# Performance work log

Measured on AMD Instinct MI355X. Metric: run time of the kernel, lower is better.

Reference implementation:

```python
import jax, jax.numpy as jnp
import numpy as np

H = 1024
NH = 16
HD = H // NH
EPS = 1e-5

def setup_inputs() -> dict:
    key = jax.random.key(0)
    ks = jax.random.split(key, 5)
    B, S = 2, 2048
    scale = 1.0 / np.sqrt(H)
    return {
        "x": jax.random.normal(ks[0], (B, S, H), dtype=jnp.float32),
        "Wq": jax.random.normal(ks[1], (H, H), dtype=jnp.float32) * scale,
        "Wk": jax.random.normal(ks[2], (H, H), dtype=jnp.float32) * scale,
        "Wv": jax.random.normal(ks[3], (H, H), dtype=jnp.float32) * scale,
        "Wo": jax.random.normal(ks[4], (H, H), dtype=jnp.float32) * scale,
        "bo": jnp.zeros((H,), dtype=jnp.float32),
        "gamma": jnp.ones((H,), dtype=jnp.float32),
        "beta": jnp.zeros((H,), dtype=jnp.float32),
    }

def reference(x, Wq, Wk, Wv, Wo, bo, gamma, beta):
    B, S, _ = x.shape
    residual = x
    # pre-LayerNorm
    mu = jnp.mean(x, axis=-1, keepdims=True)
    var = jnp.mean(jnp.square(x - mu), axis=-1, keepdims=True)
    xn = (x - mu) * jax.lax.rsqrt(var + EPS) * gamma + beta
    # QKV projections (torch Linear: y = x @ W.T), split heads -> [B, NH, S, HD]
    q = (xn @ Wq.T).reshape(B, S, NH, HD).transpose(0, 2, 1, 3)
    k = (xn @ Wk.T).reshape(B, S, NH, HD).transpose(0, 2, 1, 3)
    v = (xn @ Wv.T).reshape(B, S, NH, HD).transpose(0, 2, 1, 3)
    # naive attention: explicit [B, NH, S, S] scores
    scale = 1.0 / np.sqrt(HD)
    scores = jnp.einsum('bhqd,bhkd->bhqk', q, k) * scale
    attn = jax.nn.softmax(scores.astype(jnp.float32), axis=-1).astype(q.dtype)
    out = jnp.einsum('bhqk,bhkd->bhqd', attn, v)
    out = out.transpose(0, 2, 1, 3).reshape(B, S, H)
    out = out @ Wo.T + bo
    return out + residual
```

## Files before the change

### kernel.cpp

```cpp
#include <hip/hip_runtime.h>
#include <hip/hip_bf16.h>

#define H 1024
#define NHEAD 16
#define HDIM 64
#define SEQ 2048
#define BATCH 2
#define M_TOT (BATCH * SEQ)
#define NQKV 3072

typedef __attribute__((ext_vector_type(8))) short bf16x8;
typedef __attribute__((ext_vector_type(4))) float f32x4;

#define C2_SCALE 0.18033688f

__device__ __forceinline__ unsigned short f2bf(float f) {
  union { float f; unsigned int u; } a;
  a.f = f;
  unsigned int u = a.u;
  return (unsigned short)((u + 0x7fffu + ((u >> 16) & 1u)) >> 16);
}

__device__ __forceinline__ unsigned int pkbf(float a, float b) {
  union { __hip_bfloat162 h; unsigned int u; } cv;
  cv.h = __float22bfloat162_rn(float2{a, b});
  return cv.u;
}

__device__ __forceinline__ float fast_exp2(float x) {
#if defined(__has_builtin) && __has_builtin(__builtin_amdgcn_exp2f)
  return __builtin_amdgcn_exp2f(x);
#else
  return exp2f(x);
#endif
}

typedef const __attribute__((address_space(1))) void* gas1_t;
typedef __attribute__((address_space(3))) void* las3_t;
__device__ __forceinline__ void gload16(const void* g, void* l) {
  __builtin_amdgcn_global_load_lds((gas1_t)(unsigned long long)g,
                                   (las3_t)(unsigned int)(unsigned long long)l,
                                   16, 0, 0);
}

__global__ __launch_bounds__(256) void ln_cast_kernel(const float* __restrict__ x,
                                                      const float* __restrict__ gamma,
                                                      const float* __restrict__ beta,
                                                      unsigned short* __restrict__ xn,
                                                      const float* __restrict__ w0,
                                                      const float* __restrict__ w1,
                                                      const float* __restrict__ w2,
                                                      const float* __restrict__ w3,
                                                      unsigned short* __restrict__ wdst) {
  const int t = threadIdx.x;
  if (blockIdx.x >= M_TOT) {
    const int cb = blockIdx.x - M_TOT;
    const int y = cb >> 10;
    const float* s = (y == 0) ? w0 : (y == 1) ? w1 : (y == 2) ? w2 : w3;
    const int i = (cb & 1023) * 256 + t;
    const float4 v = ((const float4*)s)[i];
    ushort4 o;
    o.x = f2bf(v.x);
    o.y = f2bf(v.y);
    o.z = f2bf(v.z);
    o.w = f2bf(v.w);
    ((ushort4*)(wdst + (size_t)y * H * H))[i] = o;
    return;
  }
  const int row = blockIdx.x;
  const float* xr = x + (size_t)row * H;
  float4 v = ((const float4*)xr)[t];
  float s = v.x + v.y + v.z + v.w;
  float s2 = v.x * v.x + v.y * v.y + v.z * v.z + v.w * v.w;
#pragma unroll
  for (int o = 32; o; o >>= 1) {
    s += __shfl_xor(s, o, 64);
    s2 += __shfl_xor(s2, o, 64);
  }
  __shared__ float red[8];
  const int wave = t >> 6;
  if ((t & 63) == 0) {
    red[wave] = s;
    red[wave + 4] = s2;
  }
  __syncthreads();
  const float ts = red[0] + red[1] + red[2] + red[3];
  const float ts2 = red[4] + red[5] + red[6] + red[7];
  const float mu = ts * (1.0f / (float)H);
  const float var = ts2 * (1.0f / (float)H) - mu * mu;
  const float rstd = rsqrtf(var + 1e-5f);
  const float4 g = ((const float4*)gamma)[t];
  const float4 b = ((const float4*)beta)[t];
  ushort4 o;
  o.x = f2bf((v.x - mu) * rstd * g.x + b.x);
  o.y = f2bf((v.y - mu) * rstd * g.y + b.y);
  o.z = f2bf((v.z - mu) * rstd * g.z + b.z);
  o.w = f2bf((v.w - mu) * rstd * g.w + b.w);
  ((ushort4*)(xn + (size_t)row * H))[t] = o;
}

template <int EPI>
__global__ __launch_bounds__(256, 4) void gemm128(const unsigned short* __restrict__ A,
                                                  const unsigned short* __restrict__ W,
                                                  unsigned short* __restrict__ qk,
                                                  unsigned short* __restrict__ vt,
                                                  const float* __restrict__ bo,
                                                  const float* __restrict__ x,
                                                  float* __restrict__ out) {
  const int m0 = blockIdx.x * 128;
  const int n0 = blockIdx.y * 128;
  const int tid = threadIdx.x;
  const int wave = tid >> 6;
  const int lane = tid & 63;
  const int l16 = lane & 15;
  const int quad = lane >> 4;
  const int wx = wave & 1, wy = wave >> 1;

  __shared__ __align__(16) unsigned short As[2][128 * 32];
  __shared__ __align__(16) unsigned short Bs[2][128 * 32];

  const int sub = lane >> 2;
  const int kcol = (lane & 3) * 8;
  const unsigned short* ag = A + (size_t)(m0 + wave * 32 + sub) * H + kcol;
  const unsigned short* bg = W + (size_t)(n0 + wave * 32 + sub) * H + kcol;
  const int lofs = wave * 32 * 32;

  f32x4 acc[4][4] = {};

  gload16(ag, &As[0][lofs]);
  gload16(ag + 16 * H, &As[0][lofs + 16 * 32]);
  gload16(bg, &Bs[0][lofs]);
  gload16(bg + 16 * H, &Bs[0][lofs + 16 * 32]);

  for (int it = 0; it < H / 32; it++) {
    const int bi = it & 1;
    __syncthreads();
    if (it + 1 < H / 32) {
      const int k1 = (it + 1) * 32;
      gload16(ag + k1, &As[bi ^ 1][lofs]);
      gload16(ag + k1 + 16 * H, &As[bi ^ 1][lofs + 16 * 32]);
      gload16(bg + k1, &Bs[bi ^ 1][lofs]);
      gload16(bg + k1 + 16 * H, &Bs[bi ^ 1][lofs + 16 * 32]);
    }
    bf16x8 af[4], bf[4];
#pragma unroll
    for (int t = 0; t < 4; t++) {
      af[t] = *(const bf16x8*)&As[bi][(wy * 64 + t * 16 + l16) * 32 + quad * 8];
      bf[t] = *(const bf16x8*)&Bs[bi][(wx * 64 + t * 16 + l16) * 32 + quad * 8];
    }
#pragma unroll
    for (int i = 0; i < 4; i++)
#pragma unroll
      for (int j = 0; j < 4; j++)
        acc[i][j] = __builtin_amdgcn_mfma_f32_16x16x32_bf16(af[i], bf[j], acc[i][j], 0, 0, 0);
  }

  if (EPI == 0) {
#pragma unroll
    for (int j = 0; j < 4; j++) {
      const int cb = n0 + wx * 64 + j * 16;
      if (cb < 2048) {
        const float qs = (cb < 1024) ? C2_SCALE : 1.0f;
#pragma unroll
        for (int i = 0; i < 4; i++) {
          const int row = m0 + wy * 64 + i * 16 + quad * 4;
#pragma unroll
          for (int r = 0; r < 4; r++)
            qk[(size_t)(row + r) * 2048 + cb + l16] = f2bf(acc[i][j][r] * qs);
        }
      } else {
        const int n = cb + l16 - 2048;
#pragma unroll
        for (int i = 0; i < 4; i++) {
          const int row0 = m0 + wy * 64 + i * 16 + quad * 4;
          const int b = row0 >> 11;
          const int s = row0 & 2047;
          ushort4 p;
          p.x = f2bf(acc[i][j][0]);
          p.y = f2bf(acc[i][j][1]);
          p.z = f2bf(acc[i][j][2]);
          p.w = f2bf(acc[i][j][3]);
          *(ushort4*)&vt[((size_t)b * 1024 + n) * SEQ + s] = p;
        }
      }
    }
  } else {
#pragma unroll
    for (int j = 0; j < 4; j++) {
      const int col = n0 + wx * 64 + j * 16 + l16;
      const float bv = bo[col];
#pragma unroll
      for (int i = 0; i < 4; i++) {
        const int row = m0 + wy * 64 + i * 16 + quad * 4;
#pragma unroll
        for (int r = 0; r < 4; r++) {
          const size_t idx = (size_t)(row + r) * H + col;
          out[idx] = acc[i][j][r] + bv + x[idx];
        }
      }
    }
  }
}

__global__ __launch_bounds__(256, 4) void attn_kernel(const unsigned short* __restrict__ qk,
                                                      const unsigned short* __restrict__ vt,
                                                      unsigned short* __restrict__ O) {
  const int qt = blockIdx.x;
  const int h = blockIdx.y;
  const int b = blockIdx.z;
  const int tid = threadIdx.x;
  const int wave = tid >> 6;
  const int lane = tid & 63;
  const int l16 = lane & 15;
  const int quad = lane >> 4;
  const int l8 = l16 & 7;

  __shared__ __align__(16) unsigned short Kt[2][64 * 64];
  __shared__ __align__(16) unsigned short Vt[2][64 * 64];
  __shared__ __align__(16) unsigned short Pt[4][16 * 64];

  const unsigned short* Qbase = qk + (size_t)b * SEQ * 2048 + h * 64;
  const unsigned short* Kbase = qk + (size_t)b * SEQ * 2048 + 1024 + h * 64;
  const unsigned short* Vbase = vt + ((size_t)b * 1024 + h * 64) * SEQ;

  const int rIn = lane >> 3;
  const int gsw = (lane & 7) ^ rIn;
  const int ch0 = 2 * wave;

  const int qrow = qt * 64 + wave * 16 + l16;
  bf16x8 aq[2];
  aq[0] = *(const bf16x8*)(Qbase + (size_t)qrow * 2048 + quad * 8);
  aq[1] = *(const bf16x8*)(Qbase + (size_t)qrow * 2048 + 32 + quad * 8);

  float l_i = 0.0f;
  f32x4 o_acc[4] = {};

#pragma unroll
  for (int c = 0; c < 2; c++) {
    const int ch = ch0 + c;
    const int row = ch * 8 + rIn;
    gload16(Kbase + (size_t)row * 2048 + gsw * 8, &Kt[0][ch * 512]);
    gload16(Vbase + (size_t)row * SEQ + gsw * 8, &Vt[0][ch * 512]);
  }

  unsigned short* myP = &Pt[wave][0];

  for (int it = 0; it < SEQ / 64; it++) {
    const int bi = it & 1;
    __syncthreads();
    if (it + 1 < SEQ / 64) {
#pragma unroll
      for (int c = 0; c < 2; c++) {
        const int ch = ch0 + c;
        const int row = ch * 8 + rIn;
        gload16(Kbase + (size_t)((it + 1) * 64 + row) * 2048 + gsw * 8,
                &Kt[bi ^ 1][ch * 512]);
        gload16(Vbase + (size_t)row * SEQ + (it + 1) * 64 + gsw * 8,
                &Vt[bi ^ 1][ch * 512]);
      }
    }

    f32x4 s[4] = {};
#pragma unroll
    for (int c = 0; c < 2; c++) {
#pragma unroll
      for (int t = 0; t < 4; t++) {
        const bf16x8 kf =
            *(const bf16x8*)&Kt[bi][(t * 16 + l16) * 64 + (((c * 4 + quad) ^ l8) * 8)];
        s[t] = __builtin_amdgcn_mfma_f32_16x16x32_bf16(kf, aq[c], s[t], 0, 0, 0);
      }
    }

    float pv[4][4];
#pragma unroll
    for (int t = 0; t < 4; t++)
#pragma unroll
      for (int r = 0; r < 4; r++) {
        const float p = fast_exp2(s[t][r]);
        pv[t][r] = p;
        l_i += p;
      }

#pragma unroll
    for (int t = 0; t < 4; t++) {
      uint2 d;
      d.x = pkbf(pv[t][0], pv[t][1]);
      d.y = pkbf(pv[t][2], pv[t][3]);
      *(uint2*)&myP[l16 * 64 + (((t * 2 + (quad >> 1)) ^ l8) * 8) + (quad & 1) * 4] = d;
    }

#pragma unroll
    for (int c = 0; c < 2; c++) {
      const bf16x8 pb = *(const bf16x8*)&myP[l16 * 64 + (((c * 4 + quad) ^ l8) * 8)];
#pragma unroll
      for (int dt = 0; dt < 4; dt++) {
        const bf16x8 vf =
            *(const bf16x8*)&Vt[bi][(dt * 16 + l16) * 64 + (((c * 4 + quad) ^ l8) * 8)];
        o_acc[dt] = __builtin_amdgcn_mfma_f32_16x16x32_bf16(vf, pb, o_acc[dt], 0, 0, 0);
      }
    }
  }

  l_i += __shfl_xor(l_i, 16, 64);
  l_i += __shfl_xor(l_i, 32, 64);
  const float inv = 1.0f / l_i;
  unsigned short* orow = O + ((size_t)(b * SEQ + qrow)) * H + h * 64;
#pragma unroll
  for (int dt = 0; dt < 4; dt++) {
    uint2 d;
    d.x = pkbf(o_acc[dt][0] * inv, o_acc[dt][1] * inv);
    d.y = pkbf(o_acc[dt][2] * inv, o_acc[dt][3] * inv);
    *(uint2*)&orow[dt * 16 + quad * 4] = d;
  }
}

extern "C" void kernel_launch(void* const* d_in, const int* in_sizes, int n_in,
                              void* d_out, int out_size, void* d_ws, size_t ws_size,
                              hipStream_t stream) {
  const float* x = (const float*)d_in[0];
  const float* Wq = (const float*)d_in[1];
  const float* Wk = (const float*)d_in[2];
  const float* Wv = (const float*)d_in[3];
  const float* Wo = (const float*)d_in[4];
  const float* bo = (const float*)d_in[5];
  const float* gamma = (const float*)d_in[6];
  const float* beta = (const float*)d_in[7];
  float* out = (float*)d_out;

  unsigned short* ws = (unsigned short*)d_ws;
  unsigned short* xn = ws;
  unsigned short* wcat = xn + (size_t)M_TOT * H;
  unsigned short* wob = wcat + (size_t)3 * H * H;
  unsigned short* qkb = wcat + (size_t)4 * H * H;
  unsigned short* vtb = qkb + (size_t)M_TOT * 2048;
  unsigned short* atb = vtb + (size_t)BATCH * H * SEQ;

  ln_cast_kernel<<<M_TOT + 4096, 256, 0, stream>>>(x, gamma, beta, xn, Wq, Wk, Wv, Wo,
                                                   wcat);
  gemm128<0><<<dim3(M_TOT / 128, NQKV / 128), 256, 0, stream>>>(
      xn, wcat, qkb, vtb, nullptr, nullptr, nullptr);
  attn_kernel<<<dim3(SEQ / 64, NHEAD, BATCH), 256, 0, stream>>>(qkb, vtb, atb);
  gemm128<1><<<dim3(M_TOT / 128, H / 128), 256, 0, stream>>>(
      atb, wob, nullptr, nullptr, bo, x, out);
}
```

Before: 195.8 us.

## Use 32x32x16 MFMA in projection GEMMs and split attention row-sum accumulation

The 128x128 GEMM now uses 32x32x16 bf16 MFMA instructions on each wave's 64x64 sub-tile, with the shared-memory layout changed to two 16-wide k-chunks and the epilogues remapped to the 32x32 accumulator layout. Launch bounds drop to 3 blocks per SM to make room for the larger accumulators. In attention, the softmax denominator is summed into four independent partial sums instead of one serial chain, and the key loop is unrolled by two to expose more ILP. Lower occupancy and possible LDS bank conflicts in the new layout are the main risks.

```diff
diff --git a/kernel.cpp b/kernel.cpp
--- a/kernel.cpp
+++ b/kernel.cpp
@@ -11,6 +11,7 @@
 
 typedef __attribute__((ext_vector_type(8))) short bf16x8;
 typedef __attribute__((ext_vector_type(4))) float f32x4;
+typedef __attribute__((ext_vector_type(16))) float f32x16;
 
 #define C2_SCALE 0.18033688f
 
@@ -100,7 +101,7 @@
 }
 
 template <int EPI>
-__global__ __launch_bounds__(256, 4) void gemm128(const unsigned short* __restrict__ A,
+__global__ __launch_bounds__(256, 3) void gemm128(const unsigned short* __restrict__ A,
                                                   const unsigned short* __restrict__ W,
                                                   unsigned short* __restrict__ qk,
                                                   unsigned short* __restrict__ vt,
@@ -112,92 +113,101 @@
   const int tid = threadIdx.x;
   const int wave = tid >> 6;
   const int lane = tid & 63;
-  const int l16 = lane & 15;
-  const int quad = lane >> 4;
+  const int l32 = lane & 31;
+  const int hh = lane >> 5;
   const int wx = wave & 1, wy = wave >> 1;
 
-  __shared__ __align__(16) unsigned short As[2][128 * 32];
-  __shared__ __align__(16) unsigned short Bs[2][128 * 32];
-
-  const int sub = lane >> 2;
-  const int kcol = (lane & 3) * 8;
-  const unsigned short* ag = A + (size_t)(m0 + wave * 32 + sub) * H + kcol;
-  const unsigned short* bg = W + (size_t)(n0 + wave * 32 + sub) * H + kcol;
-  const int lofs = wave * 32 * 32;
-
-  f32x4 acc[4][4] = {};
-
-  gload16(ag, &As[0][lofs]);
-  gload16(ag + 16 * H, &As[0][lofs + 16 * 32]);
-  gload16(bg, &Bs[0][lofs]);
-  gload16(bg + 16 * H, &Bs[0][lofs + 16 * 32]);
+  __shared__ __align__(16) unsigned short As[2 * 8192];
+  __shared__ __align__(16) unsigned short Bs[2 * 8192];
+
+  const unsigned short* ag = A + (size_t)(m0 + wave * 32 + (lane >> 1)) * H + (lane & 1) * 8;
+  const unsigned short* bg = W + (size_t)(n0 + wave * 32 + (lane >> 1)) * H + (lane & 1) * 8;
+  const int lbase = wave * 512;
+
+  f32x16 acc[2][2] = {};
+
+#pragma unroll
+  for (int c = 0; c < 2; c++) {
+    gload16(ag + c * 16, &As[c * 2048 + lbase]);
+    gload16(bg + c * 16, &Bs[c * 2048 + lbase]);
+  }
 
   for (int it = 0; it < H / 32; it++) {
     const int bi = it & 1;
     __syncthreads();
     if (it + 1 < H / 32) {
       const int k1 = (it + 1) * 32;
-      gload16(ag + k1, &As[bi ^ 1][lofs]);
-      gload16(ag + k1 + 16 * H, &As[bi ^ 1][lofs + 16 * 32]);
-      gload16(bg + k1, &Bs[bi ^ 1][lofs]);
-      gload16(bg + k1 + 16 * H, &Bs[bi ^ 1][lofs + 16 * 32]);
-    }
-    bf16x8 af[4], bf[4];
-#pragma unroll
-    for (int t = 0; t < 4; t++) {
-      af[t] = *(const bf16x8*)&As[bi][(wy * 64 + t * 16 + l16) * 32 + quad * 8];
-      bf[t] = *(const bf16x8*)&Bs[bi][(wx * 64 + t * 16 + l16) * 32 + quad * 8];
-    }
-#pragma unroll
-    for (int i = 0; i < 4; i++)
-#pragma unroll
-      for (int j = 0; j < 4; j++)
-        acc[i][j] = __builtin_amdgcn_mfma_f32_16x16x32_bf16(af[i], bf[j], acc[i][j], 0, 0, 0);
+#pragma unroll
+      for (int c = 0; c < 2; c++) {
+        gload16(ag + k1 + c * 16, &As[(bi ^ 1) * 8192 + c * 2048 + lbase]);
+        gload16(bg + k1 + c * 16, &Bs[(bi ^ 1) * 8192 + c * 2048 + lbase]);
+      }
+    }
+    bf16x8 af[2][2], bf[2][2];
+#pragma unroll
+    for (int c = 0; c < 2; c++)
+#pragma unroll
+      for (int i = 0; i < 2; i++) {
+        af[c][i] = *(const bf16x8*)&As[bi * 8192 + c * 2048 +
+                                       (wy * 64 + i * 32 + l32) * 16 + hh * 8];
+        bf[c][i] = *(const bf16x8*)&Bs[bi * 8192 + c * 2048 +
+                                       (wx * 64 + i * 32 + l32) * 16 + hh * 8];
+      }
+#pragma unroll
+    for (int c = 0; c < 2; c++)
+#pragma unroll
+      for (int i = 0; i < 2; i++)
+#pragma unroll
+        for (int j = 0; j < 2; j++)
+          acc[i][j] =
+              __builtin_amdgcn_mfma_f32_32x32x16_bf16(af[c][i], bf[c][j], acc[i][j], 0, 0, 0);
   }
 
   if (EPI == 0) {
 #pragma unroll
-    for (int j = 0; j < 4; j++) {
-      const int cb = n0 + wx * 64 + j * 16;
+    for (int j = 0; j < 2; j++) {
+      const int cb = n0 + wx * 64 + j * 32;
       if (cb < 2048) {
         const float qs = (cb < 1024) ? C2_SCALE : 1.0f;
 #pragma unroll
-        for (int i = 0; i < 4; i++) {
-          const int row = m0 + wy * 64 + i * 16 + quad * 4;
-#pragma unroll
-          for (int r = 0; r < 4; r++)
-            qk[(size_t)(row + r) * 2048 + cb + l16] = f2bf(acc[i][j][r] * qs);
+        for (int i = 0; i < 2; i++)
+#pragma unroll
+          for (int r = 0; r < 16; r++) {
+            const int row = m0 + wy * 64 + i * 32 + (r & 3) + 8 * (r >> 2) + 4 * hh;
+            qk[(size_t)row * 2048 + cb + l32] = f2bf(acc[i][j][r] * qs);
+          }
+      } else {
+        const int n = cb + l32 - 2048;
+#pragma unroll
+        for (int i = 0; i < 2; i++) {
+          const int rb = m0 + wy * 64 + i * 32 + 4 * hh;
+          const int b = rb >> 11;
+          const int s0 = rb & 2047;
+#pragma unroll
+          for (int rg = 0; rg < 4; rg++) {
+            ushort4 p;
+            p.x = f2bf(acc[i][j][rg * 4 + 0]);
+            p.y = f2bf(acc[i][j][rg * 4 + 1]);
+            p.z = f2bf(acc[i][j][rg * 4 + 2]);
+            p.w = f2bf(acc[i][j][rg * 4 + 3]);
+            *(ushort4*)&vt[((size_t)b * 1024 + n) * SEQ + s0 + rg * 8] = p;
+          }
         }
-      } else {
-        const int n = cb + l16 - 2048;
-#pragma unroll
-        for (int i = 0; i < 4; i++) {
-          const int row0 = m0 + wy * 64 + i * 16 + quad * 4;
-          const int b = row0 >> 11;
-          const int s = row0 & 2047;
-          ushort4 p;
-          p.x = f2bf(acc[i][j][0]);
-          p.y = f2bf(acc[i][j][1]);
-          p.z = f2bf(acc[i][j][2]);
-          p.w = f2bf(acc[i][j][3]);
-          *(ushort4*)&vt[((size_t)b * 1024 + n) * SEQ + s] = p;
-        }
       }
     }
   } else {
 #pragma unroll
-    for (int j = 0; j < 4; j++) {
-      const int col = n0 + wx * 64 + j * 16 + l16;
+    for (int j = 0; j < 2; j++) {
+      const int col = n0 + wx * 64 + j * 32 + l32;
       const float bv = bo[col];
 #pragma unroll
-      for (int i = 0; i < 4; i++) {
-        const int row = m0 + wy * 64 + i * 16 + quad * 4;
-#pragma unroll
-        for (int r = 0; r < 4; r++) {
-          const size_t idx = (size_t)(row + r) * H + col;
+      for (int i = 0; i < 2; i++)
+#pragma unroll
+        for (int r = 0; r < 16; r++) {
+          const int row = m0 + wy * 64 + i * 32 + (r & 3) + 8 * (r >> 2) + 4 * hh;
+          const size_t idx = (size_t)row * H + col;
           out[idx] = acc[i][j][r] + bv + x[idx];
         }
-      }
     }
   }
 }
@@ -232,7 +242,7 @@
   aq[0] = *(const bf16x8*)(Qbase + (size_t)qrow * 2048 + quad * 8);
   aq[1] = *(const bf16x8*)(Qbase + (size_t)qrow * 2048 + 32 + quad * 8);
 
-  float l_i = 0.0f;
+  float lacc[4] = {0.0f, 0.0f, 0.0f, 0.0f};
   f32x4 o_acc[4] = {};
 
 #pragma unroll
@@ -245,6 +255,7 @@
 
   unsigned short* myP = &Pt[wave][0];
 
+#pragma unroll 2
   for (int it = 0; it < SEQ / 64; it++) {
     const int bi = it & 1;
     __syncthreads();
@@ -273,13 +284,11 @@
 
     float pv[4][4];
 #pragma unroll
-    for (int t = 0; t < 4; t++)
-#pragma unroll
-      for (int r = 0; r < 4; r++) {
-        const float p = fast_exp2(s[t][r]);
-        pv[t][r] = p;
-        l_i += p;
-      }
+    for (int t = 0; t < 4; t++) {
+#pragma unroll
+      for (int r = 0; r < 4; r++) pv[t][r] = fast_exp2(s[t][r]);
+      lacc[t] += (pv[t][0] + pv[t][1]) + (pv[t][2] + pv[t][3]);
+    }
 
 #pragma unroll
     for (int t = 0; t < 4; t++) {
@@ -301,6 +310,7 @@
     }
   }
 
+  float l_i = (lacc[0] + lacc[1]) + (lacc[2] + lacc[3]);
   l_i += __shfl_xor(l_i, 16, 64);
   l_i += __shfl_xor(l_i, 32, 64);
   const float inv = 1.0f / l_i;
```

Result: slower. 216.3 us (+10.5%).

## Process two 16-row query tiles per wave in attention to reuse K/V loads

Applied to the files above, without the earlier changes.

Each wave now handles 32 query rows instead of 16, so the attention block covers 128 queries and the grid halves. Every K and V fragment read from LDS feeds two MFMAs, which halves K/V global and LDS traffic per query. The cost is more registers (launch bounds drop to 2 blocks per CU), a doubled P staging buffer, and half as many blocks, which lowers occupancy and parallelism. The row-sum accumulation is also split into independent partial sums to shorten the dependency chain.

```diff
diff --git a/kernel.cpp b/kernel.cpp
--- a/kernel.cpp
+++ b/kernel.cpp
@@ -202,7 +202,7 @@
   }
 }
 
-__global__ __launch_bounds__(256, 4) void attn_kernel(const unsigned short* __restrict__ qk,
+__global__ __launch_bounds__(256, 2) void attn_kernel(const unsigned short* __restrict__ qk,
                                                       const unsigned short* __restrict__ vt,
                                                       unsigned short* __restrict__ O) {
   const int qt = blockIdx.x;
@@ -217,7 +217,7 @@
 
   __shared__ __align__(16) unsigned short Kt[2][64 * 64];
   __shared__ __align__(16) unsigned short Vt[2][64 * 64];
-  __shared__ __align__(16) unsigned short Pt[4][16 * 64];
+  __shared__ __align__(16) unsigned short Pt[8][16 * 64];
 
   const unsigned short* Qbase = qk + (size_t)b * SEQ * 2048 + h * 64;
   const unsigned short* Kbase = qk + (size_t)b * SEQ * 2048 + 1024 + h * 64;
@@ -227,13 +227,16 @@
   const int gsw = (lane & 7) ^ rIn;
   const int ch0 = 2 * wave;
 
-  const int qrow = qt * 64 + wave * 16 + l16;
-  bf16x8 aq[2];
-  aq[0] = *(const bf16x8*)(Qbase + (size_t)qrow * 2048 + quad * 8);
-  aq[1] = *(const bf16x8*)(Qbase + (size_t)qrow * 2048 + 32 + quad * 8);
-
-  float l_i = 0.0f;
-  f32x4 o_acc[4] = {};
+  const int qrow0 = qt * 128 + wave * 32 + l16;
+  bf16x8 aq[2][2];
+#pragma unroll
+  for (int u = 0; u < 2; u++)
+#pragma unroll
+    for (int c = 0; c < 2; c++)
+      aq[u][c] = *(const bf16x8*)(Qbase + (size_t)(qrow0 + u * 16) * 2048 + c * 32 + quad * 8);
+
+  float lacc[2][2] = {};
+  f32x4 o_acc[2][4] = {};
 
 #pragma unroll
   for (int c = 0; c < 2; c++) {
@@ -243,8 +246,10 @@
     gload16(Vbase + (size_t)row * SEQ + gsw * 8, &Vt[0][ch * 512]);
   }
 
-  unsigned short* myP = &Pt[wave][0];
-
+  unsigned short* myP0 = &Pt[wave * 2 + 0][0];
+  unsigned short* myP1 = &Pt[wave * 2 + 1][0];
+
+#pragma unroll 2
   for (int it = 0; it < SEQ / 64; it++) {
     const int bi = it & 1;
     __syncthreads();
@@ -260,57 +265,69 @@
       }
     }
 
-    f32x4 s[4] = {};
+    f32x4 s[2][4] = {};
 #pragma unroll
     for (int c = 0; c < 2; c++) {
 #pragma unroll
       for (int t = 0; t < 4; t++) {
         const bf16x8 kf =
             *(const bf16x8*)&Kt[bi][(t * 16 + l16) * 64 + (((c * 4 + quad) ^ l8) * 8)];
-        s[t] = __builtin_amdgcn_mfma_f32_16x16x32_bf16(kf, aq[c], s[t], 0, 0, 0);
-      }
-    }
-
-    float pv[4][4];
-#pragma unroll
-    for (int t = 0; t < 4; t++)
-#pragma unroll
-      for (int r = 0; r < 4; r++) {
-        const float p = fast_exp2(s[t][r]);
-        pv[t][r] = p;
-        l_i += p;
+        s[0][t] = __builtin_amdgcn_mfma_f32_16x16x32_bf16(kf, aq[0][c], s[0][t], 0, 0, 0);
+        s[1][t] = __builtin_amdgcn_mfma_f32_16x16x32_bf16(kf, aq[1][c], s[1][t], 0, 0, 0);
+      }
+    }
+
+    float pv[2][4][4];
+#pragma unroll
+    for (int u = 0; u < 2; u++)
+#pragma unroll
+      for (int t = 0; t < 4; t++) {
+#pragma unroll
+        for (int r = 0; r < 4; r++) pv[u][t][r] = fast_exp2(s[u][t][r]);
+        lacc[u][t & 1] += (pv[u][t][0] + pv[u][t][1]) + (pv[u][t][2] + pv[u][t][3]);
       }
 
 #pragma unroll
     for (int t = 0; t < 4; t++) {
-      uint2 d;
-      d.x = pkbf(pv[t][0], pv[t][1]);
-      d.y = pkbf(pv[t][2], pv[t][3]);
-      *(uint2*)&myP[l16 * 64 + (((t * 2 + (quad >> 1)) ^ l8) * 8) + (quad & 1) * 4] = d;
+      const int wofs = l16 * 64 + (((t * 2 + (quad >> 1)) ^ l8) * 8) + (quad & 1) * 4;
+      uint2 d0, d1;
+      d0.x = pkbf(pv[0][t][0], pv[0][t][1]);
+      d0.y = pkbf(pv[0][t][2], pv[0][t][3]);
+      d1.x = pkbf(pv[1][t][0], pv[1][t][1]);
+      d1.y = pkbf(pv[1][t][2], pv[1][t][3]);
+      *(uint2*)&myP0[wofs] = d0;
+      *(uint2*)&myP1[wofs] = d1;
     }
 
 #pragma unroll
     for (int c = 0; c < 2; c++) {
-      const bf16x8 pb = *(const bf16x8*)&myP[l16 * 64 + (((c * 4 + quad) ^ l8) * 8)];
+      const int rofs = l16 * 64 + (((c * 4 + quad) ^ l8) * 8);
+      const bf16x8 pb0 = *(const bf16x8*)&myP0[rofs];
+      const bf16x8 pb1 = *(const bf16x8*)&myP1[rofs];
 #pragma unroll
       for (int dt = 0; dt < 4; dt++) {
         const bf16x8 vf =
             *(const bf16x8*)&Vt[bi][(dt * 16 + l16) * 64 + (((c * 4 + quad) ^ l8) * 8)];
-        o_acc[dt] = __builtin_amdgcn_mfma_f32_16x16x32_bf16(vf, pb, o_acc[dt], 0, 0, 0);
-      }
-    }
-  }
-
-  l_i += __shfl_xor(l_i, 16, 64);
-  l_i += __shfl_xor(l_i, 32, 64);
-  const float inv = 1.0f / l_i;
-  unsigned short* orow = O + ((size_t)(b * SEQ + qrow)) * H + h * 64;
-#pragma unroll
-  for (int dt = 0; dt < 4; dt++) {
-    uint2 d;
-    d.x = pkbf(o_acc[dt][0] * inv, o_acc[dt][1] * inv);
-    d.y = pkbf(o_acc[dt][2] * inv, o_acc[dt][3] * inv);
-    *(uint2*)&orow[dt * 16 + quad * 4] = d;
+        o_acc[0][dt] = __builtin_amdgcn_mfma_f32_16x16x32_bf16(vf, pb0, o_acc[0][dt], 0, 0, 0);
+        o_acc[1][dt] = __builtin_amdgcn_mfma_f32_16x16x32_bf16(vf, pb1, o_acc[1][dt], 0, 0, 0);
+      }
+    }
+  }
+
+#pragma unroll
+  for (int u = 0; u < 2; u++) {
+    float l_i = lacc[u][0] + lacc[u][1];
+    l_i += __shfl_xor(l_i, 16, 64);
+    l_i += __shfl_xor(l_i, 32, 64);
+    const float inv = 1.0f / l_i;
+    unsigned short* orow = O + ((size_t)(b * SEQ + qrow0 + u * 16)) * H + h * 64;
+#pragma unroll
+    for (int dt = 0; dt < 4; dt++) {
+      uint2 d;
+      d.x = pkbf(o_acc[u][dt][0] * inv, o_acc[u][dt][1] * inv);
+      d.y = pkbf(o_acc[u][dt][2] * inv, o_acc[u][dt][3] * inv);
+      *(uint2*)&orow[dt * 16 + quad * 4] = d;
+    }
   }
 }
 
@@ -339,7 +356,7 @@
                                                    wcat);
   gemm128<0><<<dim3(M_TOT / 128, NQKV / 128), 256, 0, stream>>>(
       xn, wcat, qkb, vtb, nullptr, nullptr, nullptr);
-  attn_kernel<<<dim3(SEQ / 64, NHEAD, BATCH), 256, 0, stream>>>(qkb, vtb, atb);
+  attn_kernel<<<dim3(SEQ / 128, NHEAD, BATCH), 256, 0, stream>>>(qkb, vtb, atb);
   gemm128<1><<<dim3(M_TOT / 128, H / 128), 256, 0, stream>>>(
       atb, wob, nullptr, nullptr, bo, x, out);
 }
```

Measured after the change: 199.3 us. Within noise of the previous version (+1.8%).
